# Kernel optimization log

Hardware: AMD Instinct MI355X
Metric: run time of the kernel (lower is better)

Reference implementation:

```python
import jax, jax.numpy as jnp
import numpy as np
from jax import lax

BATCH, DIM, H, W = 2, 256, 48, 48
DI, NS, DR, K = 512, 16, 16, 4  # d_inner=2*dim, d_state, dt_rank=dim//16, 4 scan directions


def _dwconv(x, w, b, pad):
    # depthwise conv, NCHW, weight (C,1,kh,kw)
    y = lax.conv_general_dilated(x, w, (1, 1), [(pad, pad), (pad, pad)],
                                 dimension_numbers=('NCHW', 'OIHW', 'NCHW'),
                                 feature_group_count=x.shape[1])
    return y + b[None, :, None, None]


def _ss2d(x, in_w, cw, cb, xp, dtw, dtb, al, dp, lnw, lnb, ow):
    # VMamba-style SS2D: in_proj -> dwconv+SiLU -> 4-direction selective scan -> LN -> gate -> out_proj
    B, C, Hh, Ww = x.shape
    L = Hh * Ww
    xz = jnp.einsum('bchw,dc->bdhw', x, in_w)               # (B, 2*DI, H, W)
    xi, z = jnp.split(xz, 2, axis=1)
    xi = jax.nn.silu(_dwconv(xi, cw, cb, 1))
    x1 = xi.reshape(B, DI, L)                                # row-major scan order
    x2 = xi.transpose(0, 1, 3, 2).reshape(B, DI, L)          # column-major scan order
    xs = jnp.stack([x1, x2, x1[..., ::-1], x2[..., ::-1]], axis=1)  # (B,K,DI,L)
    x_dbl = jnp.einsum('bkdl,kcd->bkcl', xs, xp)             # (B,K,DR+2*NS,L)
    dts, Bs, Cs = jnp.split(x_dbl, [DR, DR + NS], axis=2)
    dts = jax.nn.softplus(jnp.einsum('bkrl,kdr->bkdl', dts, dtw) + dtb[None, :, :, None])
    A = -jnp.exp(al)                                         # (K,DI,NS)

    def step(h, inp):
        u_t, d_t, b_t, c_t = inp                             # (B,K,DI),(B,K,DI),(B,K,NS),(B,K,NS)
        h = jnp.exp(d_t[..., None] * A[None]) * h + (d_t * u_t)[..., None] * b_t[:, :, None, :]
        return h, jnp.sum(h * c_t[:, :, None, :], axis=-1)

    seq = (jnp.moveaxis(xs, -1, 0), jnp.moveaxis(dts, -1, 0),
           jnp.moveaxis(Bs, -1, 0), jnp.moveaxis(Cs, -1, 0))
    h0 = jnp.zeros((B, K, DI, NS), xs.dtype)
    _, ys = lax.scan(step, h0, seq)                          # ys: (L,B,K,DI)
    ys = jnp.moveaxis(ys, 0, -1) + xs * dp[None, :, :, None]  # (B,K,DI,L), skip term D*u

    y0 = ys[:, 0]
    y1 = ys[:, 1].reshape(B, DI, Ww, Hh).transpose(0, 1, 3, 2).reshape(B, DI, L)
    y2 = ys[:, 2, :, ::-1]
    y3 = ys[:, 3, :, ::-1].reshape(B, DI, Ww, Hh).transpose(0, 1, 3, 2).reshape(B, DI, L)
    y = (y0 + y1 + y2 + y3).reshape(B, DI, Hh, Ww).transpose(0, 2, 3, 1)  # (B,H,W,DI)
    mu = y.mean(-1, keepdims=True)
    y = (y - mu) * lax.rsqrt(((y - mu) ** 2).mean(-1, keepdims=True) + 1e-5) * lnw + lnb
    y = y * jax.nn.silu(z.transpose(0, 2, 3, 1))
    return jnp.einsum('bhwd,od->bohw', y, ow)               # (B,DIM,H,W)


def _forward(x, replk_w, replk_b, s1_in_w, s1_cw, s1_cb, s1_xp, s1_dtw, s1_dtb,
             s1_al, s1_d, s1_lnw, s1_lnb, s1_ow, qkv_w, q_w, q_b, k_w, k_b,
             dwc_w, dwc_b, cbr_w, cbr_g, cbr_b, s2_in_w, s2_cw, s2_cb, s2_xp,
             s2_dtw, s2_dtb, s2_al, s2_d, s2_lnw, s2_lnb, s2_ow):
    # replk: DilatedReparamBlock(dim,13) in deploy (merged) form + SS2D + ReLU6
    y = _dwconv(x, replk_w, replk_b, 6)
    y = _ss2d(y, s1_in_w, s1_cw, s1_cb, s1_xp, s1_dtw, s1_dtb, s1_al, s1_d, s1_lnw, s1_lnb, s1_ow)
    y = jnp.clip(y, 0.0, 6.0)                                # relu6
    q, k, v = jnp.split(jnp.einsum('bchw,oc->bohw', y, qkv_w), 3, axis=1)
    q = _dwconv(q, q_w, q_b, 1)
    k = _dwconv(k, k_w, k_b, 1)
    g = _dwconv(q + k, dwc_w, dwc_b, 1) * v
    # ChannelSSM: x * (CBR(avgpool(x)) + SS2D(x))
    y1 = jnp.einsum('bchw,oc->bohw', g.mean((2, 3), keepdims=True), cbr_w)
    y1 = jax.nn.relu(y1 * cbr_g[None, :, None, None] + cbr_b[None, :, None, None])  # BN(eval)+ReLU
    y2 = _ss2d(g, s2_in_w, s2_cw, s2_cb, s2_xp, s2_dtw, s2_dtb, s2_al, s2_d, s2_lnw, s2_lnb, s2_ow)
    return g * (y1 + y2)


def _ssm_params(key):
    ks = jax.random.split(key, 6)
    return dict(
        in_w=jax.random.normal(ks[0], (2 * DI, DIM)) * 0.02,
        cw=jax.random.normal(ks[1], (DI, 1, 3, 3)) * 0.1,
        cb=jnp.zeros((DI,)),
        xp=jax.random.normal(ks[2], (K, DR + 2 * NS, DI)) * 0.02,
        dtw=jax.random.normal(ks[3], (K, DI, DR)) * 0.02,
        dtb=jax.random.normal(ks[4], (K, DI)) * 0.1,
        al=jnp.log(jnp.broadcast_to(jnp.arange(1, NS + 1, dtype=jnp.float32), (K, DI, NS))),
        d=jnp.ones((K, DI)),
        lnw=jnp.ones((DI,)),
        lnb=jnp.zeros((DI,)),
        ow=jax.random.normal(ks[5], (DIM, DI)) * 0.02,
    )


def setup_inputs() -> dict:
    key = jax.random.key(0)
    ks = jax.random.split(key, 12)
    inp = dict(
        x=jax.random.normal(ks[0], (BATCH, DIM, H, W), dtype=jnp.float32),
        replk_w=jax.random.normal(ks[1], (DIM, 1, 13, 13)) * 0.05,
        replk_b=jnp.zeros((DIM,)),
        qkv_w=jax.random.normal(ks[2], (3 * DIM, DIM)) * 0.02,
        q_w=jax.random.normal(ks[3], (DIM, 1, 3, 3)) * 0.1,
        q_b=jnp.zeros((DIM,)),
        k_w=jax.random.normal(ks[4], (DIM, 1, 3, 3)) * 0.1,
        k_b=jnp.zeros((DIM,)),
        dwc_w=jax.random.normal(ks[5], (DIM, 1, 3, 3)) * 0.1,
        dwc_b=jnp.zeros((DIM,)),
        cbr_w=jax.random.normal(ks[6], (DIM, DIM)) * 0.02,
        cbr_g=jnp.ones((DIM,)),
        cbr_b=jnp.zeros((DIM,)),
    )
    for pfx, p in (('s1_', _ssm_params(ks[10])), ('s2_', _ssm_params(ks[11]))):
        for n, v in p.items():
            inp[pfx + n] = v
    return inp


def reference(x, replk_w, replk_b, s1_in_w, s1_cw, s1_cb, s1_xp, s1_dtw, s1_dtb,
              s1_al, s1_d, s1_lnw, s1_lnb, s1_ow, qkv_w, q_w, q_b, k_w, k_b,
              dwc_w, dwc_b, cbr_w, cbr_g, cbr_b, s2_in_w, s2_cw, s2_cb, s2_xp,
              s2_dtw, s2_dtb, s2_al, s2_d, s2_lnw, s2_lnb, s2_ow):
    return _forward(x, replk_w, replk_b, s1_in_w, s1_cw, s1_cb, s1_xp, s1_dtw, s1_dtb,
                    s1_al, s1_d, s1_lnw, s1_lnb, s1_ow, qkv_w, q_w, q_b, k_w, k_b,
                    dwc_w, dwc_b, cbr_w, cbr_g, cbr_b, s2_in_w, s2_cw, s2_cb, s2_xp,
                    s2_dtw, s2_dtb, s2_al, s2_d, s2_lnw, s2_lnb, s2_ow)
```

## Files before the change

kernel.cpp:

```cpp
#include <hip/hip_runtime.h>
#include <hip/hip_bf16.h>
#include <math.h>


constexpr int Bb  = 2;
constexpr int Cc  = 256;
constexpr int Hh  = 48;
constexpr int Wd  = 48;
constexpr int Ll  = Hh * Wd;
constexpr int DI  = 512;
constexpr int NS  = 16;
constexpr int DR  = 16;
constexpr int Kd4 = 4;
constexpr int NC  = 96;
constexpr int CL  = 24;

#define DEV __device__ __forceinline__

DEV float sigmoidf_(float x) { return 1.0f / (1.0f + __expf(-x)); }
DEV float siluf_(float x)    { return x * sigmoidf_(x); }

constexpr float LOG2E = 1.44269504088896340736f;
constexpr float LN2   = 0.69314718055994530942f;

DEV float softplus_fast(float x) {
    float e = exp2f(-fabsf(x) * LOG2E);
    return fmaxf(x, 0.0f) + LN2 * log2f(1.0f + e);
}

DEV unsigned short f2bf(float f) {
    unsigned u = __float_as_uint(f);
    unsigned r = (u + 0x7fffu + ((u >> 16) & 1u)) >> 16;
    return (unsigned short)r;
}
DEV float bf2f(unsigned short h) { return __uint_as_float(((unsigned)h) << 16); }

typedef __attribute__((ext_vector_type(8))) short bf16x8;
typedef __attribute__((ext_vector_type(4))) float f32x4;

__global__ __launch_bounds__(256) void split_bf16(const float* __restrict__ X,
                                                  unsigned short* __restrict__ hi,
                                                  unsigned short* __restrict__ lo,
                                                  int n)
{
    int i = (blockIdx.x * 256 + threadIdx.x) * 4;
    if (i >= n) return;
    float4 f = *(const float4*)(X + i);
    ushort4 h, l;
    h.x = f2bf(f.x); l.x = f2bf(f.x - bf2f(h.x));
    h.y = f2bf(f.y); l.y = f2bf(f.y - bf2f(h.y));
    h.z = f2bf(f.z); l.z = f2bf(f.z - bf2f(h.z));
    h.w = f2bf(f.w); l.w = f2bf(f.w - bf2f(h.w));
    *(ushort4*)(hi + i) = h;
    *(ushort4*)(lo + i) = l;
}

__global__ __launch_bounds__(256) void gemm_bfs(const unsigned short* __restrict__ Ahi,
                                                const unsigned short* __restrict__ Alo,
                                                int lda,
                                                const unsigned short* __restrict__ Whi,
                                                const unsigned short* __restrict__ Wlo,
                                                int ldw,
                                                float* __restrict__ C, int ldc,
                                                int M, int N, int K, int act)
{
    __shared__ unsigned short lAhi[64 * 40], lAlo[64 * 40];
    __shared__ unsigned short lWhi[64 * 40], lWlo[64 * 40];
    int bm = blockIdx.x * 64, bn = blockIdx.y * 64;
    int t = threadIdx.x;
    int w = t >> 6, lane = t & 63;
    int wrow = (w >> 1) * 32, wcol = (w & 1) * 32;
    int srow = t >> 2, skb = (t & 3) * 8;
    int frow = lane & 15, fkb = (lane >> 4) * 8;

    f32x4 acc[2][2] = {};

    for (int k0 = 0; k0 < K; k0 += 32) {
        size_t ga = (size_t)(bm + srow) * lda + k0 + skb;
        size_t gw = (size_t)(bn + srow) * ldw + k0 + skb;
        int ls = srow * 40 + skb;
        *reinterpret_cast<bf16x8*>(&lAhi[ls]) = *reinterpret_cast<const bf16x8*>(&Ahi[ga]);
        *reinterpret_cast<bf16x8*>(&lAlo[ls]) = *reinterpret_cast<const bf16x8*>(&Alo[ga]);
        *reinterpret_cast<bf16x8*>(&lWhi[ls]) = *reinterpret_cast<const bf16x8*>(&Whi[gw]);
        *reinterpret_cast<bf16x8*>(&lWlo[ls]) = *reinterpret_cast<const bf16x8*>(&Wlo[gw]);
        __syncthreads();

        bf16x8 a_hi[2], a_lo[2], b_hi[2], b_lo[2];
#pragma unroll
        for (int mi = 0; mi < 2; mi++) {
            int r = (wrow + mi * 16 + frow) * 40 + fkb;
            a_hi[mi] = *reinterpret_cast<const bf16x8*>(&lAhi[r]);
            a_lo[mi] = *reinterpret_cast<const bf16x8*>(&lAlo[r]);
        }
#pragma unroll
        for (int ni = 0; ni < 2; ni++) {
            int r = (wcol + ni * 16 + frow) * 40 + fkb;
            b_hi[ni] = *reinterpret_cast<const bf16x8*>(&lWhi[r]);
            b_lo[ni] = *reinterpret_cast<const bf16x8*>(&lWlo[r]);
        }

#pragma unroll
        for (int mi = 0; mi < 2; mi++)
#pragma unroll
            for (int ni = 0; ni < 2; ni++) {
                acc[mi][ni] = __builtin_amdgcn_mfma_f32_16x16x32_bf16(
                    a_hi[mi], b_hi[ni], acc[mi][ni], 0, 0, 0);
                acc[mi][ni] = __builtin_amdgcn_mfma_f32_16x16x32_bf16(
                    a_hi[mi], b_lo[ni], acc[mi][ni], 0, 0, 0);
                acc[mi][ni] = __builtin_amdgcn_mfma_f32_16x16x32_bf16(
                    a_lo[mi], b_hi[ni], acc[mi][ni], 0, 0, 0);
            }
        __syncthreads();
    }

    int r0 = bm + wrow + (lane >> 4) * 4;
    int c0 = bn + wcol + (lane & 15);
#pragma unroll
    for (int mi = 0; mi < 2; mi++)
#pragma unroll
        for (int ni = 0; ni < 2; ni++)
#pragma unroll
            for (int r = 0; r < 4; r++) {
                float v = acc[mi][ni][r];
                if (act == 1) v = fminf(fmaxf(v, 0.0f), 6.0f);
                C[(size_t)(r0 + mi * 16 + r) * ldc + c0 + ni * 16] = v;
            }
}

__global__ __launch_bounds__(256) void transpose_in(const float* __restrict__ x,
                                                    float* __restrict__ xT)
{
    __shared__ float tile[32][33];
    int l0 = blockIdx.x * 32, c0 = blockIdx.y * 32, b = blockIdx.z;
    int t = threadIdx.x;
    int li = t & 31, ci = t >> 5;
#pragma unroll
    for (int i = 0; i < 4; i++) {
        int cc = ci + i * 8;
        tile[cc][li] = x[((size_t)b * Cc + c0 + cc) * Ll + l0 + li];
    }
    __syncthreads();
#pragma unroll
    for (int i = 0; i < 4; i++) {
        int ll = ci + i * 8;
        xT[((size_t)b * Ll + l0 + ll) * Cc + c0 + li] = tile[li][ll];
    }
}

__global__ __launch_bounds__(256) void dwconv13_cm(const float* __restrict__ x,
                                                   const float* __restrict__ wgt,
                                                   const float* __restrict__ bias,
                                                   float* __restrict__ out)
{
    __shared__ float img[60 * 60];
    __shared__ float wsh[169];
    int c = blockIdx.x, b = blockIdx.y;
    int t = threadIdx.x;
    for (int i = t; i < 3600; i += 256) img[i] = 0.0f;
    if (t < 169) wsh[t] = wgt[(size_t)c * 169 + t];
    __syncthreads();
    const float* src = x + ((size_t)b * Cc + c) * Ll;
    for (int i = t; i < Ll; i += 256) {
        int h = i / 48, w = i - h * 48;
        img[(h + 6) * 60 + (w + 6)] = src[i];
    }
    __syncthreads();
    float bs = bias[c];
    float acc[9];
    int base[9];
#pragma unroll
    for (int k = 0; k < 9; k++) {
        acc[k] = bs;
        int l = t + k * 256;
        int h = l / 48, w = l - h * 48;
        base[k] = h * 60 + w;
    }
    for (int ky = 0; ky < 13; ky++) {
#pragma unroll
        for (int kx = 0; kx < 13; kx++) {
            float wv = wsh[ky * 13 + kx];
#pragma unroll
            for (int k = 0; k < 9; k++)
                acc[k] = fmaf(img[base[k] + ky * 60 + kx], wv, acc[k]);
        }
    }
    float* dst = out + ((size_t)b * Cc + c) * Ll;
#pragma unroll
    for (int k = 0; k < 9; k++)
        dst[t + k * 256] = acc[k];
}

__global__ __launch_bounds__(512) void conv3_silu_dual(const float* __restrict__ xz,
                                                       const float* __restrict__ cw,
                                                       const float* __restrict__ cb,
                                                       float* __restrict__ x1p,
                                                       float* __restrict__ x2p)
{
    __shared__ float wsm[DI * 9];
    int l = blockIdx.x, b = blockIdx.y;
    int h = l / Wd, w = l % Wd, d = threadIdx.x;
    for (int i = d; i < DI * 9; i += 512) wsm[i] = cw[i];
    __syncthreads();
    float acc = cb[d];
    const float* wp = wsm + d * 9;
#pragma unroll
    for (int ky = 0; ky < 3; ky++) {
        int y = h + ky - 1;
        if ((unsigned)y >= (unsigned)Hh) continue;
#pragma unroll
        for (int kx = 0; kx < 3; kx++) {
            int xx = w + kx - 1;
            if ((unsigned)xx >= (unsigned)Wd) continue;
            acc = fmaf(xz[((size_t)b * Ll + y * Wd + xx) * 1024 + d], wp[ky * 3 + kx], acc);
        }
    }
    float s = siluf_(acc);
    x1p[((size_t)b * Ll + l) * DI + d] = s;
    x2p[((size_t)b * Ll + (w * Hh + h)) * DI + d] = s;
}

__global__ __launch_bounds__(256) void gemm_xdbl(const float* __restrict__ x1p,
                                                 const float* __restrict__ x2p,
                                                 const float* __restrict__ xp,
                                                 float* __restrict__ xdbl)
{
    __shared__ float As[16][68];
    __shared__ float Ws[16][52];
    int z = blockIdx.z;
    int b = z >> 2, k = z & 3;
    const float* A = ((k & 1) ? x2p : x1p) + (size_t)b * Ll * DI;
    const float* W = xp + (size_t)k * 48 * DI;
    float* C = xdbl + (size_t)z * Ll * 48;
    int bm = blockIdx.x * 64;
    int t = threadIdx.x;
    int lm = t >> 2, lk = (t & 3) * 4;
    int tn = (t & 15) * 3, tm = (t >> 4) * 4;
    float acc[4][3] = {};
    for (int k0 = 0; k0 < DI; k0 += 16) {
        float4 av = *(const float4*)(A + (size_t)(bm + lm) * DI + k0 + lk);
        As[lk + 0][lm] = av.x; As[lk + 1][lm] = av.y; As[lk + 2][lm] = av.z; As[lk + 3][lm] = av.w;
        if (t < 192) {
            int wn = t >> 2;
            float4 wv = *(const float4*)(W + (size_t)wn * DI + k0 + lk);
            Ws[lk + 0][wn] = wv.x; Ws[lk + 1][wn] = wv.y; Ws[lk + 2][wn] = wv.z; Ws[lk + 3][wn] = wv.w;
        }
        __syncthreads();
#pragma unroll
        for (int kk = 0; kk < 16; kk++) {
            float a[4], w4[3];
#pragma unroll
            for (int i = 0; i < 4; i++) a[i] = As[kk][tm + i];
#pragma unroll
            for (int j = 0; j < 3; j++) w4[j] = Ws[kk][tn + j];
#pragma unroll
            for (int i = 0; i < 4; i++)
#pragma unroll
                for (int j = 0; j < 3; j++)
                    acc[i][j] = fmaf(a[i], w4[j], acc[i][j]);
        }
        __syncthreads();
    }
#pragma unroll
    for (int i = 0; i < 4; i++)
#pragma unroll
        for (int j = 0; j < 3; j++)
            C[(size_t)(bm + tm + i) * 48 + tn + j] = acc[i][j];
}

__global__ __launch_bounds__(512, 1) void scan_passA(const float* __restrict__ xdbl,
                                                     const float* __restrict__ x1p,
                                                     const float* __restrict__ x2p,
                                                     const float* __restrict__ dtw,
                                                     const float* __restrict__ dtb,
                                                     const float* __restrict__ al,
                                                     float* __restrict__ P,
                                                     float* __restrict__ Q)
{
    __shared__ __align__(16) float xds[CL * 48];
    int chunk = blockIdx.x;
    int bk = blockIdx.y;
    int b = bk >> 2, k = bk & 3;
    int d = threadIdx.x;
    int rowbase = (k < 2) ? chunk * CL : (Ll - CL * (chunk + 1));
    const float* src = xdbl + ((size_t)bk * Ll + rowbase) * 48;
    for (int i = d; i < CL * 48; i += 512) xds[i] = src[i];

    float w_dt[16];
    const float* dtwp = dtw + ((size_t)k * DI + d) * DR;
#pragma unroll
    for (int n = 0; n < 16; n++) w_dt[n] = dtwp[n];
    float A0L2 = -__expf(al[((size_t)k * DI + d) * NS]) * LOG2E;
    float dtb_s = dtb[k * DI + d];
    const float* xb = ((k & 1) ? x2p : x1p) + (size_t)b * Ll * DI + d;

    float Qr[16];
#pragma unroll
    for (int n = 0; n < 16; n++) Qr[n] = 0.0f;
    float sdt = 0.0f;
    __syncthreads();

    for (int tl = 0; tl < CL; tl++) {
        int tglob = chunk * CL + tl;
        int p  = (k < 2) ? tglob : (Ll - 1 - tglob);
        int rl = (k < 2) ? tl : (CL - 1 - tl);
        float xv[32];
        {
            const float4* xr4 = reinterpret_cast<const float4*>(&xds[rl * 48]);
#pragma unroll
            for (int i = 0; i < 8; i++) {
                float4 q = xr4[i];
                xv[4 * i + 0] = q.x; xv[4 * i + 1] = q.y; xv[4 * i + 2] = q.z; xv[4 * i + 3] = q.w;
            }
        }
        float u = xb[(size_t)p * DI];
        float dt0 = 0.f, dt1 = 0.f, dt2 = 0.f, dt3 = 0.f;
#pragma unroll
        for (int r = 0; r < 4; r++) {
            dt0 = fmaf(w_dt[r],      xv[r],      dt0);
            dt1 = fmaf(w_dt[r + 4],  xv[r + 4],  dt1);
            dt2 = fmaf(w_dt[r + 8],  xv[r + 8],  dt2);
            dt3 = fmaf(w_dt[r + 12], xv[r + 12], dt3);
        }
        float dt = softplus_fast(dtb_s + (dt0 + dt1) + (dt2 + dt3));
        sdt += dt;
        float du = dt * u;
        float e1 = exp2f(dt * A0L2);
        float pw = e1;
#pragma unroll
        for (int n = 0; n < 16; n++) {
            Qr[n] = fmaf(pw, Qr[n], du * xv[16 + n]);
            pw *= e1;
        }
    }
    float Ec = exp2f(sdt * A0L2);
    size_t obase = ((size_t)bk * NC + chunk) * NS * DI + d;
    float pw = Ec;
#pragma unroll
    for (int n = 0; n < 16; n++) {
        P[obase + (size_t)n * DI] = pw;
        Q[obase + (size_t)n * DI] = Qr[n];
        pw *= Ec;
    }
}

__global__ __launch_bounds__(512) void scan_passB(const float* __restrict__ P,
                                                  float* __restrict__ Q)
{
    int gid = blockIdx.x * 512 + threadIdx.x;
    int d = gid & (DI - 1);
    int n = (gid >> 9) & 15;
    int bk = gid >> 13;
    float h = 0.0f;
    for (int c = 0; c < NC; c++) {
        size_t idx = (((size_t)bk * NC + c) * NS + n) * DI + d;
        float p = P[idx], q = Q[idx];
        Q[idx] = h;
        h = fmaf(p, h, q);
    }
}

__global__ __launch_bounds__(512, 1) void scan_passC(const float* __restrict__ xdbl,
                                                     const float* __restrict__ x1p,
                                                     const float* __restrict__ x2p,
                                                     const float* __restrict__ dtw,
                                                     const float* __restrict__ dtb,
                                                     const float* __restrict__ al,
                                                     const float* __restrict__ dsk,
                                                     const float* __restrict__ hin,
                                                     float* __restrict__ ysA)
{
    __shared__ __align__(16) float xds[CL * 48];
    int chunk = blockIdx.x;
    int bk = blockIdx.y;
    int b = bk >> 2, k = bk & 3;
    int d = threadIdx.x;
    int rowbase = (k < 2) ? chunk * CL : (Ll - CL * (chunk + 1));
    const float* src = xdbl + ((size_t)bk * Ll + rowbase) * 48;
    for (int i = d; i < CL * 48; i += 512) xds[i] = src[i];

    float w_dt[16], hreg[16];
    const float* dtwp = dtw + ((size_t)k * DI + d) * DR;
#pragma unroll
    for (int n = 0; n < 16; n++) w_dt[n] = dtwp[n];
    float A0L2 = -__expf(al[((size_t)k * DI + d) * NS]) * LOG2E;
    float dtb_s = dtb[k * DI + d];
    float dp_s  = dsk[k * DI + d];
    size_t hbase = ((size_t)bk * NC + chunk) * NS * DI + d;
#pragma unroll
    for (int n = 0; n < 16; n++) hreg[n] = hin[hbase + (size_t)n * DI];
    const float* xb = ((k & 1) ? x2p : x1p) + (size_t)b * Ll * DI + d;
    __syncthreads();

    for (int tl = 0; tl < CL; tl++) {
        int tglob = chunk * CL + tl;
        int p  = (k < 2) ? tglob : (Ll - 1 - tglob);
        int rl = (k < 2) ? tl : (CL - 1 - tl);
        float xv[48];
        {
            const float4* xr4 = reinterpret_cast<const float4*>(&xds[rl * 48]);
#pragma unroll
            for (int i = 0; i < 12; i++) {
                float4 q = xr4[i];
                xv[4 * i + 0] = q.x; xv[4 * i + 1] = q.y; xv[4 * i + 2] = q.z; xv[4 * i + 3] = q.w;
            }
        }
        float u = xb[(size_t)p * DI];
        float dt0 = 0.f, dt1 = 0.f, dt2 = 0.f, dt3 = 0.f;
#pragma unroll
        for (int r = 0; r < 4; r++) {
            dt0 = fmaf(w_dt[r],      xv[r],      dt0);
            dt1 = fmaf(w_dt[r + 4],  xv[r + 4],  dt1);
            dt2 = fmaf(w_dt[r + 8],  xv[r + 8],  dt2);
            dt3 = fmaf(w_dt[r + 12], xv[r + 12], dt3);
        }
        float dt = softplus_fast(dtb_s + (dt0 + dt1) + (dt2 + dt3));
        float du = dt * u;
        float e1 = exp2f(dt * A0L2);
        float pw = e1;
        float y = 0.0f;
#pragma unroll
        for (int n = 0; n < 16; n++) {
            hreg[n] = fmaf(pw, hreg[n], du * xv[16 + n]);
            y = fmaf(hreg[n], xv[32 + n], y);
            pw *= e1;
        }
        y = fmaf(dp_s, u, y);
        ysA[((size_t)bk * Ll + p) * DI + d] = y;
    }
}

__global__ __launch_bounds__(512) void combine_ln(const float* __restrict__ ysA,
                                                  const float* __restrict__ xz,
                                                  const float* __restrict__ lnw,
                                                  const float* __restrict__ lnb,
                                                  float* __restrict__ yln)
{
    __shared__ float red[16];
    int l = blockIdx.x, b = blockIdx.y;
    int h = l / Wd, w = l % Wd;
    int wh = w * Hh + h;
    int d = threadIdx.x;
    size_t k0 = ((size_t)(b * 4 + 0) * Ll + l)  * DI + d;
    size_t k1 = ((size_t)(b * 4 + 1) * Ll + wh) * DI + d;
    size_t k2 = ((size_t)(b * 4 + 2) * Ll + l)  * DI + d;
    size_t k3 = ((size_t)(b * 4 + 3) * Ll + wh) * DI + d;
    float v = ysA[k0] + ysA[k1] + ysA[k2] + ysA[k3];

    float s = v, s2 = v * v;
#pragma unroll
    for (int off = 32; off > 0; off >>= 1) {
        s  += __shfl_down(s, off);
        s2 += __shfl_down(s2, off);
    }
    int wid = d >> 6, lane = d & 63;
    if (lane == 0) { red[wid] = s; red[8 + wid] = s2; }
    __syncthreads();
    if (d == 0) {
        float ts = 0.0f, ts2 = 0.0f;
        for (int i = 0; i < 8; i++) { ts += red[i]; ts2 += red[8 + i]; }
        red[0] = ts * (1.0f / DI);
        red[1] = ts2 * (1.0f / DI);
    }
    __syncthreads();
    float mu = red[0];
    float var = red[1] - mu * mu;
    float yn = (v - mu) * rsqrtf(var + 1e-5f) * lnw[d] + lnb[d];
    float zv = xz[((size_t)b * Ll + l) * 1024 + DI + d];
    yn *= siluf_(zv);
    yln[((size_t)b * Ll + l) * DI + d] = yn;
}

__global__ __launch_bounds__(256) void conv_qk(const float* __restrict__ qkv,
                                               const float* __restrict__ qw,
                                               const float* __restrict__ qb,
                                               const float* __restrict__ kw,
                                               const float* __restrict__ kb,
                                               float* __restrict__ sbuf)
{
    __shared__ float wq[Cc * 9], wk[Cc * 9];
    int l = blockIdx.x, b = blockIdx.y;
    int h = l / Wd, w = l % Wd, c = threadIdx.x;
    for (int i = c; i < Cc * 9; i += 256) { wq[i] = qw[i]; wk[i] = kw[i]; }
    __syncthreads();
    float aq = qb[c], ak = kb[c];
#pragma unroll
    for (int ky = 0; ky < 3; ky++) {
        int y = h + ky - 1;
        if ((unsigned)y >= (unsigned)Hh) continue;
#pragma unroll
        for (int kx = 0; kx < 3; kx++) {
            int xx = w + kx - 1;
            if ((unsigned)xx >= (unsigned)Wd) continue;
            size_t base = ((size_t)b * Ll + y * Wd + xx) * 768;
            aq = fmaf(qkv[base + c],       wq[c * 9 + ky * 3 + kx], aq);
            ak = fmaf(qkv[base + Cc + c],  wk[c * 9 + ky * 3 + kx], ak);
        }
    }
    sbuf[((size_t)b * Ll + l) * Cc + c] = aq + ak;
}

__global__ __launch_bounds__(256) void conv_g(const float* __restrict__ sbuf,
                                              const float* __restrict__ dw,
                                              const float* __restrict__ db,
                                              const float* __restrict__ qkv,
                                              float* __restrict__ g)
{
    __shared__ float wsm[Cc * 9];
    int l = blockIdx.x, b = blockIdx.y;
    int h = l / Wd, w = l % Wd, c = threadIdx.x;
    for (int i = c; i < Cc * 9; i += 256) wsm[i] = dw[i];
    __syncthreads();
    float acc = db[c];
#pragma unroll
    for (int ky = 0; ky < 3; ky++) {
        int y = h + ky - 1;
        if ((unsigned)y >= (unsigned)Hh) continue;
#pragma unroll
        for (int kx = 0; kx < 3; kx++) {
            int xx = w + kx - 1;
            if ((unsigned)xx >= (unsigned)Wd) continue;
            acc = fmaf(sbuf[((size_t)b * Ll + y * Wd + xx) * Cc + c], wsm[c * 9 + ky * 3 + kx], acc);
        }
    }
    float v = qkv[((size_t)b * Ll + l) * 768 + 2 * Cc + c];
    g[((size_t)b * Ll + l) * Cc + c] = acc * v;
}

__global__ __launch_bounds__(256) void reduce_mean(const float* __restrict__ g,
                                                   float* __restrict__ m)
{
    int b = blockIdx.y, c = threadIdx.x;
    int l0 = blockIdx.x * 128;
    float s = 0.0f;
    for (int i = 0; i < 128; i++)
        s += g[((size_t)b * Ll + l0 + i) * Cc + c];
    atomicAdd(&m[b * Cc + c], s);
}

__global__ __launch_bounds__(256) void cbr_kernel(const float* __restrict__ m,
                                                  const float* __restrict__ wgt,
                                                  const float* __restrict__ gain,
                                                  const float* __restrict__ bias,
                                                  float* __restrict__ y1)
{
    __shared__ float ms[Cc];
    int b = blockIdx.x, o = threadIdx.x;
    ms[o] = m[b * Cc + o] * (1.0f / (float)Ll);
    __syncthreads();
    float t = 0.0f;
    for (int c = 0; c < Cc; c++) t = fmaf(ms[c], wgt[(size_t)o * Cc + c], t);
    float v = t * gain[o] + bias[o];
    y1[b * Cc + o] = fmaxf(v, 0.0f);
}

__global__ __launch_bounds__(256) void final_kernel(const float* __restrict__ g,
                                                    const float* __restrict__ y1,
                                                    const float* __restrict__ y2,
                                                    float* __restrict__ out)
{
    __shared__ float tile[32][33];
    int l0 = blockIdx.x * 32, o0 = blockIdx.y * 32, b = blockIdx.z;
    int t = threadIdx.x;
    int lo = t & 31, li = t >> 5;
#pragma unroll
    for (int i = 0; i < 4; i++) {
        int ll = li + i * 8;
        size_t idx = ((size_t)b * Ll + l0 + ll) * Cc + o0 + lo;
        tile[ll][lo] = g[idx] * (y1[b * Cc + o0 + lo] + y2[idx]);
    }
    __syncthreads();
#pragma unroll
    for (int i = 0; i < 4; i++) {
        int oo = li + i * 8;
        out[((size_t)b * Cc + o0 + oo) * Ll + l0 + lo] = tile[lo][oo];
    }
}

struct SSParams {
    const float *in_w, *cw, *cb, *xp, *dtw, *dtb, *al, *dsk, *lnw, *lnb, *ow;
};

static void run_ss2d(const float* inp, const SSParams& p, float* outp, int act,
                     float* xz, float* x1p, float* x2p, float* xdbl,
                     float* Pb, float* Qb, float* ysA, float* yln,
                     hipStream_t stream)
{
    const int Mrows = Bb * Ll;
    unsigned short* awhi = (unsigned short*)Pb;
    unsigned short* awlo = awhi + 2359296;
    unsigned short* wwhi = (unsigned short*)Qb;
    unsigned short* wwlo = wwhi + 262144;

    split_bf16<<<dim3((2 * DI * Cc) / 1024), 256, 0, stream>>>(p.in_w, wwhi, wwlo, 2 * DI * Cc);
    split_bf16<<<dim3((Mrows * Cc) / 1024), 256, 0, stream>>>(inp, awhi, awlo, Mrows * Cc);
    gemm_bfs<<<dim3(Mrows / 64, 1024 / 64), 256, 0, stream>>>(awhi, awlo, Cc, wwhi, wwlo, Cc,
                                                              xz, 1024, Mrows, 1024, Cc, 0);
    conv3_silu_dual<<<dim3(Ll, Bb), 512, 0, stream>>>(xz, p.cw, p.cb, x1p, x2p);
    gemm_xdbl<<<dim3(Ll / 64, 1, Bb * Kd4), 256, 0, stream>>>(x1p, x2p, p.xp, xdbl);
    scan_passA<<<dim3(NC, Bb * Kd4), 512, 0, stream>>>(xdbl, x1p, x2p, p.dtw, p.dtb, p.al, Pb, Qb);
    scan_passB<<<dim3((Bb * Kd4 * NS * DI) / 512), 512, 0, stream>>>(Pb, Qb);
    scan_passC<<<dim3(NC, Bb * Kd4), 512, 0, stream>>>(xdbl, x1p, x2p, p.dtw, p.dtb, p.al,
                                                       p.dsk, Qb, ysA);
    combine_ln<<<dim3(Ll, Bb), 512, 0, stream>>>(ysA, xz, p.lnw, p.lnb, yln);
    split_bf16<<<dim3((Mrows * DI) / 1024), 256, 0, stream>>>(yln, awhi, awlo, Mrows * DI);
    split_bf16<<<dim3((Cc * DI) / 1024), 256, 0, stream>>>(p.ow, wwhi, wwlo, Cc * DI);
    gemm_bfs<<<dim3(Mrows / 64, Cc / 64), 256, 0, stream>>>(awhi, awlo, DI, wwhi, wwlo, DI,
                                                            outp, Cc, Mrows, Cc, DI, act);
}

extern "C" void kernel_launch(void* const* d_in, const int* in_sizes, int n_in,
                              void* d_out, int out_size, void* d_ws, size_t ws_size,
                              hipStream_t stream)
{
    int i_x, i_rw, i_rb, i_qkv, i_qw, i_qb, i_kw, i_kb, i_dw, i_db, i_cw, i_cg, i_cb2, s1b, s2b;
    if (in_sizes[3] == 3 * 256 * 256) {
        i_x = 0; i_rw = 1; i_rb = 2; i_qkv = 3; i_qw = 4; i_qb = 5; i_kw = 6; i_kb = 7;
        i_dw = 8; i_db = 9; i_cw = 10; i_cg = 11; i_cb2 = 12; s1b = 13; s2b = 24;
    } else {
        i_x = 0; i_rw = 1; i_rb = 2; s1b = 3; i_qkv = 14; i_qw = 15; i_qb = 16; i_kw = 17;
        i_kb = 18; i_dw = 19; i_db = 20; i_cw = 21; i_cg = 22; i_cb2 = 23; s2b = 24;
    }
    auto F = [&](int i) { return (const float*)d_in[i]; };
    const float* x      = F(i_x);
    const float* replkw = F(i_rw);
    const float* replkb = F(i_rb);
    const float* qkvw   = F(i_qkv);
    const float* qw     = F(i_qw);
    const float* qb     = F(i_qb);
    const float* kw     = F(i_kw);
    const float* kb     = F(i_kb);
    const float* dww    = F(i_dw);
    const float* dwb    = F(i_db);
    const float* cbrw   = F(i_cw);
    const float* cbrg   = F(i_cg);
    const float* cbrb   = F(i_cb2);
    SSParams s1 { F(s1b+0), F(s1b+1), F(s1b+2), F(s1b+3), F(s1b+4), F(s1b+5),
                  F(s1b+6), F(s1b+7), F(s1b+8), F(s1b+9), F(s1b+10) };
    SSParams s2 { F(s2b+0), F(s2b+1), F(s2b+2), F(s2b+3), F(s2b+4), F(s2b+5),
                  F(s2b+6), F(s2b+7), F(s2b+8), F(s2b+9), F(s2b+10) };

    float* ws = (float*)d_ws;
    size_t off = 0;
    auto alloc = [&](size_t n) { float* p = ws + off; off += n; return p; };
    float* ycm  = alloc((size_t)Bb * Ll * Cc);
    float* yrep = alloc((size_t)Bb * Ll * Cc);
    float* xz   = alloc((size_t)Bb * Ll * 1024);
    float* x1p  = alloc((size_t)Bb * Ll * DI);
    float* x2p  = alloc((size_t)Bb * Ll * DI);
    float* xdbl = alloc((size_t)Bb * Kd4 * Ll * 48);
    float* Pb   = alloc((size_t)Bb * Kd4 * NC * NS * DI);
    float* Qb   = alloc((size_t)Bb * Kd4 * NC * NS * DI);
    float* ysA  = alloc((size_t)Bb * Kd4 * Ll * DI);
    float* yln  = alloc((size_t)Bb * Ll * DI);
    float* s1o  = alloc((size_t)Bb * Ll * Cc);
    float* qkvb = alloc((size_t)Bb * Ll * 768);
    float* gbuf = alloc((size_t)Bb * Ll * Cc);
    float* mbuf = alloc((size_t)Bb * Cc);
    float* y1b  = alloc((size_t)Bb * Cc);
    float* sbuf = yrep;
    float* y2b  = ycm;
    (void)ws_size; (void)n_in; (void)out_size;

    const int Mrows = Bb * Ll;
    unsigned short* awhi = (unsigned short*)Pb;
    unsigned short* awlo = awhi + 2359296;
    unsigned short* wwhi = (unsigned short*)Qb;
    unsigned short* wwlo = wwhi + 262144;

    dwconv13_cm<<<dim3(Cc, Bb), 256, 0, stream>>>(x, replkw, replkb, ycm);
    transpose_in<<<dim3(Ll / 32, Cc / 32, Bb), 256, 0, stream>>>(ycm, yrep);
    run_ss2d(yrep, s1, s1o, 1, xz, x1p, x2p, xdbl, Pb, Qb, ysA, yln, stream);
    split_bf16<<<dim3((768 * Cc) / 1024), 256, 0, stream>>>(qkvw, wwhi, wwlo, 768 * Cc);
    split_bf16<<<dim3((Mrows * Cc) / 1024), 256, 0, stream>>>(s1o, awhi, awlo, Mrows * Cc);
    gemm_bfs<<<dim3(Mrows / 64, 768 / 64), 256, 0, stream>>>(awhi, awlo, Cc, wwhi, wwlo, Cc,
                                                             qkvb, 768, Mrows, 768, Cc, 0);
    conv_qk<<<dim3(Ll, Bb), 256, 0, stream>>>(qkvb, qw, qb, kw, kb, sbuf);
    conv_g<<<dim3(Ll, Bb), 256, 0, stream>>>(sbuf, dww, dwb, qkvb, gbuf);
    (void)hipMemsetAsync(mbuf, 0, (size_t)Bb * Cc * sizeof(float), stream);
    reduce_mean<<<dim3(Ll / 128, Bb), 256, 0, stream>>>(gbuf, mbuf);
    cbr_kernel<<<dim3(Bb), 256, 0, stream>>>(mbuf, cbrw, cbrg, cbrb, y1b);
    run_ss2d(gbuf, s2, y2b, 0, xz, x1p, x2p, xdbl, Pb, Qb, ysA, yln, stream);
    final_kernel<<<dim3(Ll / 32, Cc / 32, Bb), 256, 0, stream>>>(gbuf, y1b, y2b, (float*)d_out);
}
```

Measured before the change: 585.5 us.

## Fuse bf16 hi/lo split into MFMA GEMM loads and use MFMA for x_dbl projection

Removes the separate split_bf16 kernels by converting fp32 operands to bf16 hi/lo pairs inside the GEMM tile load, which saves the extra global round trips and launches. The x_dbl projection, previously a scalar fp32 LDS GEMM, now runs on the same split-bf16 MFMA body, with row clamping and column masking for N=48. In exchange, every block redoes the conversion of each tile, and the fp32 loads are twice the size of the old bf16 loads.

```diff
diff --git a/kernel.cpp b/kernel.cpp
--- a/kernel.cpp
+++ b/kernel.cpp
@@ -38,51 +38,48 @@
 typedef __attribute__((ext_vector_type(8))) short bf16x8;
 typedef __attribute__((ext_vector_type(4))) float f32x4;
 
-__global__ __launch_bounds__(256) void split_bf16(const float* __restrict__ X,
-                                                  unsigned short* __restrict__ hi,
-                                                  unsigned short* __restrict__ lo,
-                                                  int n)
-{
-    int i = (blockIdx.x * 256 + threadIdx.x) * 4;
-    if (i >= n) return;
-    float4 f = *(const float4*)(X + i);
-    ushort4 h, l;
-    h.x = f2bf(f.x); l.x = f2bf(f.x - bf2f(h.x));
-    h.y = f2bf(f.y); l.y = f2bf(f.y - bf2f(h.y));
-    h.z = f2bf(f.z); l.z = f2bf(f.z - bf2f(h.z));
-    h.w = f2bf(f.w); l.w = f2bf(f.w - bf2f(h.w));
-    *(ushort4*)(hi + i) = h;
-    *(ushort4*)(lo + i) = l;
-}
-
-__global__ __launch_bounds__(256) void gemm_bfs(const unsigned short* __restrict__ Ahi,
-                                                const unsigned short* __restrict__ Alo,
-                                                int lda,
-                                                const unsigned short* __restrict__ Whi,
-                                                const unsigned short* __restrict__ Wlo,
-                                                int ldw,
-                                                float* __restrict__ C, int ldc,
-                                                int M, int N, int K, int act)
-{
-    __shared__ unsigned short lAhi[64 * 40], lAlo[64 * 40];
-    __shared__ unsigned short lWhi[64 * 40], lWlo[64 * 40];
-    int bm = blockIdx.x * 64, bn = blockIdx.y * 64;
+DEV void gemm_mfma_body(const float* __restrict__ A, int lda,
+                        const float* __restrict__ W, int ldw,
+                        float* __restrict__ C, int ldc,
+                        int bm, int bn, int K, int Wrows, int Nstore, int act,
+                        unsigned short* lds)
+{
+    unsigned short* lAhi = lds;
+    unsigned short* lAlo = lds + 2560;
+    unsigned short* lWhi = lds + 5120;
+    unsigned short* lWlo = lds + 7680;
     int t = threadIdx.x;
     int w = t >> 6, lane = t & 63;
     int wrow = (w >> 1) * 32, wcol = (w & 1) * 32;
     int srow = t >> 2, skb = (t & 3) * 8;
     int frow = lane & 15, fkb = (lane >> 4) * 8;
+    int wr = bn + srow; if (wr > Wrows - 1) wr = Wrows - 1;
 
     f32x4 acc[2][2] = {};
 
     for (int k0 = 0; k0 < K; k0 += 32) {
         size_t ga = (size_t)(bm + srow) * lda + k0 + skb;
-        size_t gw = (size_t)(bn + srow) * ldw + k0 + skb;
+        size_t gw = (size_t)wr * ldw + k0 + skb;
+        float av[8], wv[8];
+        *(float4*)&av[0] = *(const float4*)(A + ga);
+        *(float4*)&av[4] = *(const float4*)(A + ga + 4);
+        *(float4*)&wv[0] = *(const float4*)(W + gw);
+        *(float4*)&wv[4] = *(const float4*)(W + gw + 4);
+        bf16x8 ah, al, wh, wl;
+#pragma unroll
+        for (int j = 0; j < 8; j++) {
+            unsigned short h = f2bf(av[j]);
+            ah[j] = (short)h;
+            al[j] = (short)f2bf(av[j] - bf2f(h));
+            unsigned short hw = f2bf(wv[j]);
+            wh[j] = (short)hw;
+            wl[j] = (short)f2bf(wv[j] - bf2f(hw));
+        }
         int ls = srow * 40 + skb;
-        *reinterpret_cast<bf16x8*>(&lAhi[ls]) = *reinterpret_cast<const bf16x8*>(&Ahi[ga]);
-        *reinterpret_cast<bf16x8*>(&lAlo[ls]) = *reinterpret_cast<const bf16x8*>(&Alo[ga]);
-        *reinterpret_cast<bf16x8*>(&lWhi[ls]) = *reinterpret_cast<const bf16x8*>(&Whi[gw]);
-        *reinterpret_cast<bf16x8*>(&lWlo[ls]) = *reinterpret_cast<const bf16x8*>(&Wlo[gw]);
+        *reinterpret_cast<bf16x8*>(&lAhi[ls]) = ah;
+        *reinterpret_cast<bf16x8*>(&lAlo[ls]) = al;
+        *reinterpret_cast<bf16x8*>(&lWhi[ls]) = wh;
+        *reinterpret_cast<bf16x8*>(&lWlo[ls]) = wl;
         __syncthreads();
 
         bf16x8 a_hi[2], a_lo[2], b_hi[2], b_lo[2];
@@ -121,10 +118,36 @@
         for (int ni = 0; ni < 2; ni++)
 #pragma unroll
             for (int r = 0; r < 4; r++) {
+                int col = c0 + ni * 16;
+                if (col >= Nstore) continue;
                 float v = acc[mi][ni][r];
                 if (act == 1) v = fminf(fmaxf(v, 0.0f), 6.0f);
-                C[(size_t)(r0 + mi * 16 + r) * ldc + c0 + ni * 16] = v;
+                C[(size_t)(r0 + mi * 16 + r) * ldc + col] = v;
             }
+}
+
+__global__ __launch_bounds__(256) void gemm_f32s(const float* __restrict__ A, int lda,
+                                                 const float* __restrict__ W, int ldw,
+                                                 float* __restrict__ C, int ldc,
+                                                 int K, int N, int act)
+{
+    __shared__ unsigned short lds[10240];
+    gemm_mfma_body(A, lda, W, ldw, C, ldc, blockIdx.x * 64, blockIdx.y * 64,
+                   K, N, N, act, lds);
+}
+
+__global__ __launch_bounds__(256) void gemm_xdbl_mfma(const float* __restrict__ x1p,
+                                                      const float* __restrict__ x2p,
+                                                      const float* __restrict__ xp,
+                                                      float* __restrict__ xdbl)
+{
+    __shared__ unsigned short lds[10240];
+    int z = blockIdx.z;
+    int b = z >> 2, k = z & 3;
+    const float* A = ((k & 1) ? x2p : x1p) + (size_t)b * Ll * DI;
+    const float* W = xp + (size_t)k * 48 * DI;
+    float* C = xdbl + (size_t)z * Ll * 48;
+    gemm_mfma_body(A, DI, W, DI, C, 48, blockIdx.x * 64, 0, DI, 48, 48, 0, lds);
 }
 
 __global__ __launch_bounds__(256) void transpose_in(const float* __restrict__ x,
@@ -217,54 +240,6 @@
     float s = siluf_(acc);
     x1p[((size_t)b * Ll + l) * DI + d] = s;
     x2p[((size_t)b * Ll + (w * Hh + h)) * DI + d] = s;
-}
-
-__global__ __launch_bounds__(256) void gemm_xdbl(const float* __restrict__ x1p,
-                                                 const float* __restrict__ x2p,
-                                                 const float* __restrict__ xp,
-                                                 float* __restrict__ xdbl)
-{
-    __shared__ float As[16][68];
-    __shared__ float Ws[16][52];
-    int z = blockIdx.z;
-    int b = z >> 2, k = z & 3;
-    const float* A = ((k & 1) ? x2p : x1p) + (size_t)b * Ll * DI;
-    const float* W = xp + (size_t)k * 48 * DI;
-    float* C = xdbl + (size_t)z * Ll * 48;
-    int bm = blockIdx.x * 64;
-    int t = threadIdx.x;
-    int lm = t >> 2, lk = (t & 3) * 4;
-    int tn = (t & 15) * 3, tm = (t >> 4) * 4;
-    float acc[4][3] = {};
-    for (int k0 = 0; k0 < DI; k0 += 16) {
-        float4 av = *(const float4*)(A + (size_t)(bm + lm) * DI + k0 + lk);
-        As[lk + 0][lm] = av.x; As[lk + 1][lm] = av.y; As[lk + 2][lm] = av.z; As[lk + 3][lm] = av.w;
-        if (t < 192) {
-            int wn = t >> 2;
-            float4 wv = *(const float4*)(W + (size_t)wn * DI + k0 + lk);
-            Ws[lk + 0][wn] = wv.x; Ws[lk + 1][wn] = wv.y; Ws[lk + 2][wn] = wv.z; Ws[lk + 3][wn] = wv.w;
-        }
-        __syncthreads();
-#pragma unroll
-        for (int kk = 0; kk < 16; kk++) {
-            float a[4], w4[3];
-#pragma unroll
-            for (int i = 0; i < 4; i++) a[i] = As[kk][tm + i];
-#pragma unroll
-            for (int j = 0; j < 3; j++) w4[j] = Ws[kk][tn + j];
-#pragma unroll
-            for (int i = 0; i < 4; i++)
-#pragma unroll
-                for (int j = 0; j < 3; j++)
-                    acc[i][j] = fmaf(a[i], w4[j], acc[i][j]);
-        }
-        __syncthreads();
-    }
-#pragma unroll
-    for (int i = 0; i < 4; i++)
-#pragma unroll
-        for (int j = 0; j < 3; j++)
-            C[(size_t)(bm + tm + i) * 48 + tn + j] = acc[i][j];
 }
 
 __global__ __launch_bounds__(512, 1) void scan_passA(const float* __restrict__ xdbl,
@@ -586,26 +561,17 @@
                      hipStream_t stream)
 {
     const int Mrows = Bb * Ll;
-    unsigned short* awhi = (unsigned short*)Pb;
-    unsigned short* awlo = awhi + 2359296;
-    unsigned short* wwhi = (unsigned short*)Qb;
-    unsigned short* wwlo = wwhi + 262144;
-
-    split_bf16<<<dim3((2 * DI * Cc) / 1024), 256, 0, stream>>>(p.in_w, wwhi, wwlo, 2 * DI * Cc);
-    split_bf16<<<dim3((Mrows * Cc) / 1024), 256, 0, stream>>>(inp, awhi, awlo, Mrows * Cc);
-    gemm_bfs<<<dim3(Mrows / 64, 1024 / 64), 256, 0, stream>>>(awhi, awlo, Cc, wwhi, wwlo, Cc,
-                                                              xz, 1024, Mrows, 1024, Cc, 0);
+    gemm_f32s<<<dim3(Mrows / 64, 1024 / 64), 256, 0, stream>>>(inp, Cc, p.in_w, Cc,
+                                                               xz, 1024, Cc, 1024, 0);
     conv3_silu_dual<<<dim3(Ll, Bb), 512, 0, stream>>>(xz, p.cw, p.cb, x1p, x2p);
-    gemm_xdbl<<<dim3(Ll / 64, 1, Bb * Kd4), 256, 0, stream>>>(x1p, x2p, p.xp, xdbl);
+    gemm_xdbl_mfma<<<dim3(Ll / 64, 1, Bb * Kd4), 256, 0, stream>>>(x1p, x2p, p.xp, xdbl);
     scan_passA<<<dim3(NC, Bb * Kd4), 512, 0, stream>>>(xdbl, x1p, x2p, p.dtw, p.dtb, p.al, Pb, Qb);
     scan_passB<<<dim3((Bb * Kd4 * NS * DI) / 512), 512, 0, stream>>>(Pb, Qb);
     scan_passC<<<dim3(NC, Bb * Kd4), 512, 0, stream>>>(xdbl, x1p, x2p, p.dtw, p.dtb, p.al,
                                                        p.dsk, Qb, ysA);
     combine_ln<<<dim3(Ll, Bb), 512, 0, stream>>>(ysA, xz, p.lnw, p.lnb, yln);
-    split_bf16<<<dim3((Mrows * DI) / 1024), 256, 0, stream>>>(yln, awhi, awlo, Mrows * DI);
-    split_bf16<<<dim3((Cc * DI) / 1024), 256, 0, stream>>>(p.ow, wwhi, wwlo, Cc * DI);
-    gemm_bfs<<<dim3(Mrows / 64, Cc / 64), 256, 0, stream>>>(awhi, awlo, DI, wwhi, wwlo, DI,
-                                                            outp, Cc, Mrows, Cc, DI, act);
+    gemm_f32s<<<dim3(Mrows / 64, Cc / 64), 256, 0, stream>>>(yln, DI, p.ow, DI,
+                                                             outp, Cc, DI, Cc, act);
 }
 
 extern "C" void kernel_launch(void* const* d_in, const int* in_sizes, int n_in,
@@ -662,18 +628,12 @@
     (void)ws_size; (void)n_in; (void)out_size;
 
     const int Mrows = Bb * Ll;
-    unsigned short* awhi = (unsigned short*)Pb;
-    unsigned short* awlo = awhi + 2359296;
-    unsigned short* wwhi = (unsigned short*)Qb;
-    unsigned short* wwlo = wwhi + 262144;
 
     dwconv13_cm<<<dim3(Cc, Bb), 256, 0, stream>>>(x, replkw, replkb, ycm);
     transpose_in<<<dim3(Ll / 32, Cc / 32, Bb), 256, 0, stream>>>(ycm, yrep);
     run_ss2d(yrep, s1, s1o, 1, xz, x1p, x2p, xdbl, Pb, Qb, ysA, yln, stream);
-    split_bf16<<<dim3((768 * Cc) / 1024), 256, 0, stream>>>(qkvw, wwhi, wwlo, 768 * Cc);
-    split_bf16<<<dim3((Mrows * Cc) / 1024), 256, 0, stream>>>(s1o, awhi, awlo, Mrows * Cc);
-    gemm_bfs<<<dim3(Mrows / 64, 768 / 64), 256, 0, stream>>>(awhi, awlo, Cc, wwhi, wwlo, Cc,
-                                                             qkvb, 768, Mrows, 768, Cc, 0);
+    gemm_f32s<<<dim3(Mrows / 64, 768 / 64), 256, 0, stream>>>(s1o, Cc, qkvw, Cc,
+                                                              qkvb, 768, Cc, 768, 0);
     conv_qk<<<dim3(Ll, Bb), 256, 0, stream>>>(qkvb, qw, qb, kw, kb, sbuf);
     conv_g<<<dim3(Ll, Bb), 256, 0, stream>>>(sbuf, dww, dwb, qkvb, gbuf);
     (void)hipMemsetAsync(mbuf, 0, (size_t)Bb * Cc * sizeof(float), stream);
```

After: 529.9 us. 1.1x faster.
